# Kernel optimization log

Hardware: AMD Instinct MI355X
Metric: run time of the kernel (lower is better)

The kernel has to match this reference:

```python
import jax, jax.numpy as jnp
import numpy as np

NUM_HEADS = 8
MASK_RATE = 0.5


def setup_inputs() -> dict:
    key = jax.random.key(0)
    ks = jax.random.split(key, 6)
    B, N, C = 8, 1024, 256
    TABLE = 10
    att_embedding = jax.random.normal(ks[0], (B, N, C), dtype=jnp.float32)
    relation_position = jax.random.randint(ks[1], (B, N, N), 0, TABLE, dtype=jnp.int32)
    rel_len = jax.random.randint(ks[2], (B,), 0, 20, dtype=jnp.int32)
    W_qkv = jax.random.normal(ks[3], (C, 3 * C), dtype=jnp.float32) * (1.0 / np.sqrt(C))
    W_proj = jax.random.normal(ks[4], (C, C), dtype=jnp.float32) * (1.0 / np.sqrt(C))
    b_proj = jnp.zeros((C,), dtype=jnp.float32)
    bias_table = jax.random.normal(ks[5], (TABLE, NUM_HEADS), dtype=jnp.float32) * 0.02
    return {
        "att_embedding": att_embedding,
        "relation_position": relation_position,
        "rel_len": rel_len,
        "W_qkv": W_qkv,
        "W_proj": W_proj,
        "b_proj": b_proj,
        "bias_table": bias_table,
    }


def reference(att_embedding, relation_position, rel_len, W_qkv, W_proj, b_proj, bias_table):
    B, N, C = att_embedding.shape
    H = NUM_HEADS
    hd = C // H
    scale = hd ** -0.5

    # QKV projection (no bias): [B,N,3C] -> q,k,v each [B,H,N,hd]
    qkv = (att_embedding @ W_qkv).reshape(B, N, 3, H, hd)
    qkv = jnp.transpose(qkv, (2, 0, 3, 1, 4))
    q, k, v = qkv[0], qkv[1], qkv[2]

    # Attention scores [B,H,N,N]
    attn = jnp.einsum("bhnd,bhmd->bhnm", q, k) * scale

    # Relative position bias: gather [B,N,N,H] -> [B,H,N,N]
    pos_bias = jnp.transpose(bias_table[relation_position], (0, 3, 1, 2))

    # Mask bias: table row t gets -100 iff t > mask_len (mask_len+1 .. TABLE-1);
    # identical across heads -> compute as [B,1,N,N] instead of materializing [B,H,N,N].
    mask_len = (rel_len.astype(jnp.float32) * MASK_RATE).astype(jnp.int32)
    mask_bias = jnp.where(relation_position > mask_len[:, None, None], -100.0, 0.0)[:, None]

    attn = jax.nn.softmax(attn + pos_bias + mask_bias, axis=-1)

    # Weighted values -> [B,N,C] -> output projection
    x = jnp.einsum("bhnm,bhmd->bnhd", attn, v).reshape(B, N, C)
    x = x @ W_proj + b_proj
    return x
```

## Files before the change

kernel.cpp:

```cpp
#include <hip/hip_runtime.h>
#include <hip/hip_bf16.h>

typedef __bf16 bf16;
typedef __bf16 bf16x2 __attribute__((ext_vector_type(2)));
typedef __bf16 bf16x8 __attribute__((ext_vector_type(8)));
typedef float f32x4 __attribute__((ext_vector_type(4)));
typedef int i32x4 __attribute__((ext_vector_type(4)));

#define B_ 8
#define N_ 1024
#define C_ 256
#define H_ 8
#define C3_ 768
#define SCALE 0.17677669529663689f
#define FMAX 16.0f


__global__ __launch_bounds__(256) void prep(
    const float* __restrict__ Wqkv, const float* __restrict__ Wproj,
    bf16* __restrict__ Wq_tiled, bf16* __restrict__ Wp_tiled)
{
  int bb = blockIdx.x;
  int o = bb * 256 + threadIdx.x;
  if (bb < 768) {
    int kk = o & 31;
    int idx = o >> 5;
    int nr = idx & 63;
    int qq = idx >> 6;
    int nt = qq % 12, kt = qq / 12;
    int n = nt * 64 + nr, k = kt * 32 + kk;
    Wq_tiled[o] = (bf16)Wqkv[k * C3_ + n];
  } else {
    int p = o - 768 * 256;
    int kk = p & 31;
    int n = (p >> 5) & 255;
    int kt = p >> 13;
    int k = kt * 32 + kk;
    Wp_tiled[p] = (bf16)Wproj[k * C_ + n];
  }
}

__global__ __launch_bounds__(256) void gemm_qkv(
    const float* __restrict__ A, const bf16* __restrict__ Wq_tiled,
    bf16* __restrict__ q, bf16* __restrict__ kT, bf16* __restrict__ vT)
{
  __shared__ bf16 As[128][40];
  __shared__ bf16 Bts[128][40];
  __shared__ bf16 Vls[64][136];

  int tid = threadIdx.x;
  int wave = tid >> 6, lane = tid & 63, quad = lane >> 4, l16 = lane & 15;
  int m0 = blockIdx.x * 128, n0 = blockIdx.y * 128;
  int msub = (wave & 1) * 64, nsub = (wave >> 1) * 64;

  f32x4 acc[4][4] = {};

  int arow = tid >> 1, akc = (tid & 1) * 16;
  const float* aptr = A + (long)(m0 + arow) * C_ + akc;
  int bn = tid >> 1, bkc = (tid & 1) * 16;
  const bf16* bptr = Wq_tiled +
      ((long)(blockIdx.y * 2 + (bn >> 6)) * 2048 + (bn & 63) * 32 + bkc);

  float4 a0 = *reinterpret_cast<const float4*>(aptr);
  float4 a1 = *reinterpret_cast<const float4*>(aptr + 4);
  float4 a2 = *reinterpret_cast<const float4*>(aptr + 8);
  float4 a3 = *reinterpret_cast<const float4*>(aptr + 12);
  i32x4 bv0 = *reinterpret_cast<const i32x4*>(bptr);
  i32x4 bv1 = *reinterpret_cast<const i32x4*>(bptr + 8);

  for (int kt = 0; kt < 8; ++kt) {
    __syncthreads();
    {
      bf16 at[16] = {(bf16)a0.x, (bf16)a0.y, (bf16)a0.z, (bf16)a0.w,
                     (bf16)a1.x, (bf16)a1.y, (bf16)a1.z, (bf16)a1.w,
                     (bf16)a2.x, (bf16)a2.y, (bf16)a2.z, (bf16)a2.w,
                     (bf16)a3.x, (bf16)a3.y, (bf16)a3.z, (bf16)a3.w};
      *reinterpret_cast<bf16x8*>(&As[arow][akc]) = *reinterpret_cast<bf16x8*>(at);
      *reinterpret_cast<bf16x8*>(&As[arow][akc + 8]) = *reinterpret_cast<bf16x8*>(at + 8);
      *reinterpret_cast<i32x4*>(&Bts[bn][bkc]) = bv0;
      *reinterpret_cast<i32x4*>(&Bts[bn][bkc + 8]) = bv1;
    }
    __syncthreads();

    if (kt < 7) {
      int kn = (kt + 1) * 32;
      a0 = *reinterpret_cast<const float4*>(aptr + kn);
      a1 = *reinterpret_cast<const float4*>(aptr + kn + 4);
      a2 = *reinterpret_cast<const float4*>(aptr + kn + 8);
      a3 = *reinterpret_cast<const float4*>(aptr + kn + 12);
      bv0 = *reinterpret_cast<const i32x4*>(bptr + (long)(kt + 1) * 24576);
      bv1 = *reinterpret_cast<const i32x4*>(bptr + (long)(kt + 1) * 24576 + 8);
    }

    bf16x8 af[4], bfr[4];
#pragma unroll
    for (int mi = 0; mi < 4; ++mi)
      af[mi] = *reinterpret_cast<const bf16x8*>(&As[msub + mi * 16 + l16][quad * 8]);
#pragma unroll
    for (int ni = 0; ni < 4; ++ni)
      bfr[ni] = *reinterpret_cast<const bf16x8*>(&Bts[nsub + ni * 16 + l16][quad * 8]);
#pragma unroll
    for (int mi = 0; mi < 4; ++mi)
#pragma unroll
      for (int ni = 0; ni < 4; ++ni)
        acc[mi][ni] = __builtin_amdgcn_mfma_f32_16x16x32_bf16(af[mi], bfr[ni], acc[mi][ni], 0, 0, 0);
  }

  if (n0 < 256) {
#pragma unroll
    for (int mi = 0; mi < 4; ++mi)
#pragma unroll
      for (int ni = 0; ni < 4; ++ni)
#pragma unroll
        for (int r = 0; r < 4; ++r) {
          int row = m0 + msub + mi * 16 + quad * 4 + r;
          int col = n0 + nsub + ni * 16 + l16;
          q[(long)row * 256 + col] = (bf16)(acc[mi][ni][r] * SCALE);
        }
  } else if (n0 < 512) {
#pragma unroll
    for (int mi = 0; mi < 4; ++mi)
#pragma unroll
      for (int ni = 0; ni < 4; ++ni)
#pragma unroll
        for (int r = 0; r < 4; ++r) {
          int row = m0 + msub + mi * 16 + quad * 4 + r;
          int c = n0 + nsub + ni * 16 + l16 - 256;
          int b = row >> 10, n = row & 1023;
          int h = c >> 5, d = c & 31;
          kT[(((long)(b * H_ + h)) * N_ + n) * 32 + d] = (bf16)acc[mi][ni][r];
        }
  } else {
    int b = m0 >> 10;
#pragma unroll
    for (int ch = 0; ch < 2; ++ch) {
      __syncthreads();
      if ((nsub >> 6) == ch) {
#pragma unroll
        for (int mi = 0; mi < 4; ++mi)
#pragma unroll
          for (int ni = 0; ni < 4; ++ni)
#pragma unroll
            for (int r = 0; r < 4; ++r) {
              int cc = ni * 16 + l16;
              int nn = msub + mi * 16 + quad * 4 + r;
              int np = (nn & 96) | ((nn & 12) << 1) | (nn & 3) | (((nn >> 4) & 1) << 2);
              Vls[cc][np] = (bf16)acc[mi][ni][r];
            }
      }
      __syncthreads();
      int cc = tid >> 2, nseg = (tid & 3) * 32;
      long base = ((long)(b * C_ + (n0 - 512) + ch * 64 + cc)) * N_ + (m0 & 1023) + nseg;
#pragma unroll
      for (int j = 0; j < 4; ++j)
        *reinterpret_cast<i32x4*>(vT + base + j * 8) =
            *reinterpret_cast<const i32x4*>(&Vls[cc][nseg + j * 8]);
    }
  }
}

__global__ __launch_bounds__(512) void flash_attn(
    const bf16* __restrict__ q, const bf16* __restrict__ kT,
    const bf16* __restrict__ vT, const int* __restrict__ rel,
    const int* __restrict__ rel_len, const float* __restrict__ btab,
    const bf16* __restrict__ Wp_tiled, const float* __restrict__ bias,
    float* __restrict__ out)
{
  __shared__ __align__(16) char smem[74240];
  char* KBp = smem;
  char* VBp = smem + 32768;
  char* RBp = smem + 65536;
  float* ebtl = (float*)(smem + 73728);

  int tid = threadIdx.x;
  int h = tid >> 6, lane = tid & 63, quad = lane >> 4, l16 = lane & 15;

  int wg = blockIdx.y * 64 + blockIdx.x;
  int swz = (wg & 7) * 64 + (wg >> 3);
  int b = swz >> 6, i0 = (swz & 63) * 16;
  long bN = (long)b * N_;

  int mask_len = (int)((float)rel_len[b] * 0.5f);
  if (tid < 80) {
    int t = tid >> 3, hh = tid & 7;
    ebtl[hh * 16 + t] = __expf(btab[t * H_ + hh] + (t > mask_len ? -100.f : 0.f) - FMAX);
  }

  bf16x8 qf = *reinterpret_cast<const bf16x8*>(
      q + (bN + i0 + l16) * 256 + h * 32 + quad * 8);

  int l = lane;
  int sxc = (((l & 3) ^ ((l >> 3) & 3)) << 4);
  int kc0 = (l >> 2) * 64 + sxc;
  int vc0 = (h * 32 + (l >> 2)) * 2048 + sxc;
  int i_loc = (h & 3) * 4 + (l >> 4);
  int j_loc = (h >> 2) * 16 + ((((l >> 2) & 3) ^ ((i_loc >> 1) & 3)) << 2) + (l & 3);
  int rc = i_loc * 4096 + j_loc * 4;

  const char* kTb = (const char*)kT + ((long)(b * 8 + h) << 16);
  const char* vTb = (const char*)vT + (long)b * 524288;
  const char* rb0 = (const char*)rel + (bN + i0) * 4096;

  int swq = ((quad ^ ((l16 >> 1) & 3)) << 4);
  int kr = h * 2048 + l16 * 64 + swq;
  int rr = l16 * 64 + swq;

#define GLD16(G, L) __builtin_amdgcn_global_load_lds(                         \
    (const __attribute__((address_space(1))) void*)(G),                       \
    (__attribute__((address_space(3))) void*)(L), 16, 0, 0)
#define GLD4(G, L) __builtin_amdgcn_global_load_lds(                          \
    (const __attribute__((address_space(1))) void*)(G),                       \
    (__attribute__((address_space(3))) void*)(L), 4, 0, 0)

#define GATH(G, R0, R1) do {                                                  \
    _Pragma("unroll")                                                         \
    for (int e = 0; e < 4; ++e) {                                             \
      G[e]     = ebtl[h * 16 + R0[e]];                                        \
      G[4 + e] = ebtl[h * 16 + R1[e]];                                        \
    }                                                                         \
  } while (0)

#define COMP(K0, K1, V0, V1, G) do {                                          \
    f32x4 z = {};                                                             \
    f32x4 s0 = __builtin_amdgcn_mfma_f32_16x16x32_bf16(K0, qf, z, 0, 0, 0);   \
    f32x4 s1 = __builtin_amdgcn_mfma_f32_16x16x32_bf16(K1, qf, z, 0, 0, 0);   \
    bf16x8 pa;                                                                \
    _Pragma("unroll")                                                         \
    for (int e = 0; e < 4; ++e) {                                             \
      float p0 = __expf(s0[e]) * G[e];                                        \
      float p1 = __expf(s1[e]) * G[4 + e];                                    \
      l_acc += p0 + p1;                                                       \
      pa[e] = (bf16)p0;                                                       \
      pa[4 + e] = (bf16)p1;                                                   \
    }                                                                         \
    oacc[0] = __builtin_amdgcn_mfma_f32_16x16x32_bf16(pa, V0, oacc[0], 0, 0, 0); \
    oacc[1] = __builtin_amdgcn_mfma_f32_16x16x32_bf16(pa, V1, oacc[1], 0, 0, 0); \
  } while (0)

#define TILE(TT, BC, BN, BRN, BR3, GC, GN) do {                               \
    int tn_ = ((TT) + 1) & 31, tr_ = ((TT) + 3) & 31;                         \
    GLD16(kTb + tn_ * 2048 + kc0,       KBp + (BN) * 16384 + h * 2048);       \
    GLD16(kTb + tn_ * 2048 + kc0 + 1024, KBp + (BN) * 16384 + h * 2048 + 1024);\
    GLD16(vTb + tn_ * 64 + vc0,         VBp + (BN) * 16384 + h * 2048);       \
    GLD16(vTb + tn_ * 64 + vc0 + 32768, VBp + (BN) * 16384 + h * 2048 + 1024);\
    GLD4(rb0 + tr_ * 128 + rc,          RBp + (BR3) * 2048 + h * 256);        \
    asm volatile("s_waitcnt vmcnt(6)" ::: "memory");                          \
    __builtin_amdgcn_s_barrier();                                             \
    bf16x8 kf0 = *(const bf16x8*)(KBp + (BC) * 16384 + kr);                   \
    bf16x8 kf1 = *(const bf16x8*)(KBp + (BC) * 16384 + kr + 1024);            \
    bf16x8 vf0 = *(const bf16x8*)(VBp + (BC) * 16384 + kr);                   \
    bf16x8 vf1 = *(const bf16x8*)(VBp + (BC) * 16384 + kr + 1024);            \
    i32x4 rv0 = *(const i32x4*)(RBp + (BRN) * 2048 + rr);                     \
    i32x4 rv1 = *(const i32x4*)(RBp + (BRN) * 2048 + rr + 1024);              \
    GATH(GN, rv0, rv1);                                                       \
    COMP(kf0, kf1, vf0, vf1, GC);                                             \
    __builtin_amdgcn_s_barrier();                                             \
  } while (0)

  f32x4 oacc[2] = {};
  float l_acc = 0.f;
  float gA[8], gB[8];

  GLD16(kTb + kc0,        KBp + h * 2048);
  GLD16(kTb + kc0 + 1024, KBp + h * 2048 + 1024);
  GLD16(vTb + vc0,         VBp + h * 2048);
  GLD16(vTb + vc0 + 32768, VBp + h * 2048 + 1024);
  GLD4(rb0 + rc,       RBp + h * 256);
  GLD4(rb0 + 128 + rc, RBp + 2048 + h * 256);
  GLD4(rb0 + 256 + rc, RBp + 4096 + h * 256);
  asm volatile("s_waitcnt vmcnt(2)" ::: "memory");
  __syncthreads();
  {
    i32x4 rv0 = *(const i32x4*)(RBp + rr);
    i32x4 rv1 = *(const i32x4*)(RBp + rr + 1024);
    GATH(gA, rv0, rv1);
  }

#pragma unroll 1
  for (int t = 0; t < 32; t += 4) {
    TILE(t + 0, 0, 1, 1, 3, gA, gB);
    TILE(t + 1, 1, 0, 2, 0, gB, gA);
    TILE(t + 2, 0, 1, 3, 1, gA, gB);
    TILE(t + 3, 1, 0, 0, 2, gB, gA);
  }
#undef TILE
#undef COMP
#undef GATH
#undef GLD16
#undef GLD4

  asm volatile("s_waitcnt vmcnt(0)" ::: "memory");
  __syncthreads();

  float lsum = l_acc;
  lsum += __shfl_xor(lsum, 16);
  lsum += __shfl_xor(lsum, 32);
  float inv = 1.f / lsum;

  bf16 (*attL)[264] = (bf16(*)[264])(void*)smem;
#pragma unroll
  for (int r = 0; r < 4; ++r) {
    float invr = __shfl(inv, quad * 4 + r);
    attL[quad * 4 + r][h * 32 + l16] = (bf16)(oacc[0][r] * invr);
    attL[quad * 4 + r][h * 32 + 16 + l16] = (bf16)(oacc[1][r] * invr);
  }
  __syncthreads();

  f32x4 pacc[2] = {};
  const bf16* wp = Wp_tiled + ((h * 32 + l16) * 32 + quad * 8);
#pragma unroll
  for (int kt = 0; kt < 8; ++kt) {
    bf16x8 afr = *reinterpret_cast<const bf16x8*>(&attL[l16][kt * 32 + quad * 8]);
    bf16x8 b0 = *reinterpret_cast<const bf16x8*>(wp + kt * 8192);
    bf16x8 b1 = *reinterpret_cast<const bf16x8*>(wp + kt * 8192 + 512);
    pacc[0] = __builtin_amdgcn_mfma_f32_16x16x32_bf16(afr, b0, pacc[0], 0, 0, 0);
    pacc[1] = __builtin_amdgcn_mfma_f32_16x16x32_bf16(afr, b1, pacc[1], 0, 0, 0);
  }
  float bi0 = bias[h * 32 + l16];
  float bi1 = bias[h * 32 + 16 + l16];
#pragma unroll
  for (int r = 0; r < 4; ++r) {
    long rowoff = (bN + i0 + quad * 4 + r) * C_ + h * 32;
    out[rowoff + l16] = pacc[0][r] + bi0;
    out[rowoff + 16 + l16] = pacc[1][r] + bi1;
  }
}

extern "C" void kernel_launch(void* const* d_in, const int* in_sizes, int n_in,
                              void* d_out, int out_size, void* d_ws, size_t ws_size,
                              hipStream_t stream) {
  const float* X     = (const float*)d_in[0];
  const int*   rel   = (const int*)d_in[1];
  const int*   rlen  = (const int*)d_in[2];
  const float* Wqkv  = (const float*)d_in[3];
  const float* Wproj = (const float*)d_in[4];
  const float* bproj = (const float*)d_in[5];
  const float* btab  = (const float*)d_in[6];
  float* out = (float*)d_out;

  char* ws = (char*)d_ws;
  bf16* Wq_tiled = (bf16*)ws;
  bf16* Wp_tiled = (bf16*)(ws + 393216);
  bf16* q  = (bf16*)(ws + 524288);
  bf16* kT = (bf16*)(ws + 524288 + 4194304);
  bf16* vT = (bf16*)(ws + 524288 + 2 * 4194304);

  prep<<<dim3(1024), 256, 0, stream>>>(Wqkv, Wproj, Wq_tiled, Wp_tiled);
  gemm_qkv<<<dim3(8192 / 128, C3_ / 128), 256, 0, stream>>>(X, Wq_tiled, q, kT, vT);
  flash_attn<<<dim3(N_ / 16, B_), 512, 0, stream>>>(
      q, kT, vT, rel, rlen, btab, Wp_tiled, bproj, out);
}
```

Before: 136.7 us.

## Pack relation indices to bytes and drop per-tile barriers in flash attention

The prep kernel gains extra blocks that convert the int32 relation_position tensor into a uint8 copy in workspace. The attention kernel then streams one quarter of the bytes for the bias gather, unpacking indices with shifts. Its shared-memory layout is rearranged so each wave only reads the K, V and relation slices it loaded itself. That lets the two block-wide barriers per tile be removed, and the relation buffering becomes a three-slot rotation with a 6-way unrolled loop. The trade-off is an extra full read of the int32 tensor plus a byte write in the prep stage, in exchange for less traffic and less synchronisation in the main loop.

```diff
diff --git a/kernel.cpp b/kernel.cpp
--- a/kernel.cpp
+++ b/kernel.cpp
@@ -18,11 +18,13 @@
 
 __global__ __launch_bounds__(256) void prep(
     const float* __restrict__ Wqkv, const float* __restrict__ Wproj,
-    bf16* __restrict__ Wq_tiled, bf16* __restrict__ Wp_tiled)
+    const int* __restrict__ rel,
+    bf16* __restrict__ Wq_tiled, bf16* __restrict__ Wp_tiled,
+    unsigned char* __restrict__ rel8)
 {
   int bb = blockIdx.x;
-  int o = bb * 256 + threadIdx.x;
   if (bb < 768) {
+    int o = bb * 256 + threadIdx.x;
     int kk = o & 31;
     int idx = o >> 5;
     int nr = idx & 63;
@@ -30,13 +32,25 @@
     int nt = qq % 12, kt = qq / 12;
     int n = nt * 64 + nr, k = kt * 32 + kk;
     Wq_tiled[o] = (bf16)Wqkv[k * C3_ + n];
-  } else {
-    int p = o - 768 * 256;
+  } else if (bb < 1024) {
+    int p = (bb - 768) * 256 + threadIdx.x;
     int kk = p & 31;
     int n = (p >> 5) & 255;
     int kt = p >> 13;
     int k = kt * 32 + kk;
     Wp_tiled[p] = (bf16)Wproj[k * C_ + n];
+  } else {
+    long p = ((long)(bb - 1024) * 256 + threadIdx.x) * 16;
+    i32x4 a = *reinterpret_cast<const i32x4*>(rel + p);
+    i32x4 b2 = *reinterpret_cast<const i32x4*>(rel + p + 4);
+    i32x4 c = *reinterpret_cast<const i32x4*>(rel + p + 8);
+    i32x4 d = *reinterpret_cast<const i32x4*>(rel + p + 12);
+    unsigned o0 = (unsigned)a[0] | ((unsigned)a[1] << 8) | ((unsigned)a[2] << 16) | ((unsigned)a[3] << 24);
+    unsigned o1 = (unsigned)b2[0] | ((unsigned)b2[1] << 8) | ((unsigned)b2[2] << 16) | ((unsigned)b2[3] << 24);
+    unsigned o2 = (unsigned)c[0] | ((unsigned)c[1] << 8) | ((unsigned)c[2] << 16) | ((unsigned)c[3] << 24);
+    unsigned o3 = (unsigned)d[0] | ((unsigned)d[1] << 8) | ((unsigned)d[2] << 16) | ((unsigned)d[3] << 24);
+    i32x4 ov = {(int)o0, (int)o1, (int)o2, (int)o3};
+    *reinterpret_cast<i32x4*>(rel8 + p) = ov;
   }
 }
 
@@ -161,16 +175,16 @@
 
 __global__ __launch_bounds__(512) void flash_attn(
     const bf16* __restrict__ q, const bf16* __restrict__ kT,
-    const bf16* __restrict__ vT, const int* __restrict__ rel,
+    const bf16* __restrict__ vT, const unsigned char* __restrict__ rel8,
     const int* __restrict__ rel_len, const float* __restrict__ btab,
     const bf16* __restrict__ Wp_tiled, const float* __restrict__ bias,
     float* __restrict__ out)
 {
-  __shared__ __align__(16) char smem[74240];
-  char* KBp = smem;
-  char* VBp = smem + 32768;
-  char* RBp = smem + 65536;
-  float* ebtl = (float*)(smem + 73728);
+  __shared__ __align__(16) char smem[78336];
+  char* const KB0 = smem;
+  char* const VB0 = smem + 32768;
+  char* const RB0 = smem + 65536;
+  float* const ebtl = (float*)(smem + 77824);
 
   int tid = threadIdx.x;
   int h = tid >> 6, lane = tid & 63, quad = lane >> 4, l16 = lane & 15;
@@ -189,21 +203,25 @@
   bf16x8 qf = *reinterpret_cast<const bf16x8*>(
       q + (bN + i0 + l16) * 256 + h * 32 + quad * 8);
 
+  __syncthreads();
+
   int l = lane;
   int sxc = (((l & 3) ^ ((l >> 3) & 3)) << 4);
   int kc0 = (l >> 2) * 64 + sxc;
   int vc0 = (h * 32 + (l >> 2)) * 2048 + sxc;
-  int i_loc = (h & 3) * 4 + (l >> 4);
-  int j_loc = (h >> 2) * 16 + ((((l >> 2) & 3) ^ ((i_loc >> 1) & 3)) << 2) + (l & 3);
-  int rc = i_loc * 4096 + j_loc * 4;
+  int rc0 = (l >> 3) * 1024 + (l & 7) * 4;
 
   const char* kTb = (const char*)kT + ((long)(b * 8 + h) << 16);
   const char* vTb = (const char*)vT + (long)b * 524288;
-  const char* rb0 = (const char*)rel + (bN + i0) * 4096;
+  const char* rb8 = (const char*)rel8 + (bN + i0) * 1024;
 
   int swq = ((quad ^ ((l16 >> 1) & 3)) << 4);
   int kr = h * 2048 + l16 * 64 + swq;
-  int rr = l16 * 64 + swq;
+  int rr = h * 512 + l16 * 32 + quad * 4;
+
+#define KB(i) (KB0 + (i) * 16384)
+#define VB(i) (VB0 + (i) * 16384)
+#define RB(i) (RB0 + (i) * 4096)
 
 #define GLD16(G, L) __builtin_amdgcn_global_load_lds(                         \
     (const __attribute__((address_space(1))) void*)(G),                       \
@@ -212,11 +230,11 @@
     (const __attribute__((address_space(1))) void*)(G),                       \
     (__attribute__((address_space(3))) void*)(L), 4, 0, 0)
 
-#define GATH(G, R0, R1) do {                                                  \
+#define GATH(G, RV0, RV1) do {                                                \
     _Pragma("unroll")                                                         \
     for (int e = 0; e < 4; ++e) {                                             \
-      G[e]     = ebtl[h * 16 + R0[e]];                                        \
-      G[4 + e] = ebtl[h * 16 + R1[e]];                                        \
+      G[e]     = ebtl[h * 16 + (int)((RV0 >> (8 * e)) & 255u)];               \
+      G[4 + e] = ebtl[h * 16 + (int)((RV1 >> (8 * e)) & 255u)];               \
     }                                                                         \
   } while (0)
 
@@ -237,57 +255,65 @@
     oacc[1] = __builtin_amdgcn_mfma_f32_16x16x32_bf16(pa, V1, oacc[1], 0, 0, 0); \
   } while (0)
 
-#define TILE(TT, BC, BN, BRN, BR3, GC, GN) do {                               \
-    int tn_ = ((TT) + 1) & 31, tr_ = ((TT) + 3) & 31;                         \
-    GLD16(kTb + tn_ * 2048 + kc0,       KBp + (BN) * 16384 + h * 2048);       \
-    GLD16(kTb + tn_ * 2048 + kc0 + 1024, KBp + (BN) * 16384 + h * 2048 + 1024);\
-    GLD16(vTb + tn_ * 64 + vc0,         VBp + (BN) * 16384 + h * 2048);       \
-    GLD16(vTb + tn_ * 64 + vc0 + 32768, VBp + (BN) * 16384 + h * 2048 + 1024);\
-    GLD4(rb0 + tr_ * 128 + rc,          RBp + (BR3) * 2048 + h * 256);        \
-    asm volatile("s_waitcnt vmcnt(6)" ::: "memory");                          \
-    __builtin_amdgcn_s_barrier();                                             \
-    bf16x8 kf0 = *(const bf16x8*)(KBp + (BC) * 16384 + kr);                   \
-    bf16x8 kf1 = *(const bf16x8*)(KBp + (BC) * 16384 + kr + 1024);            \
-    bf16x8 vf0 = *(const bf16x8*)(VBp + (BC) * 16384 + kr);                   \
-    bf16x8 vf1 = *(const bf16x8*)(VBp + (BC) * 16384 + kr + 1024);            \
-    i32x4 rv0 = *(const i32x4*)(RBp + (BRN) * 2048 + rr);                     \
-    i32x4 rv1 = *(const i32x4*)(RBp + (BRN) * 2048 + rr + 1024);              \
+#define TILE(T_, KVR, KVW, RR_, RW_, GC, GN) do {                             \
+    int tn_ = ((T_) + 1) & 31, tr_ = ((T_) + 3) & 31;                         \
+    GLD16(kTb + tn_ * 2048 + kc0,        KB(KVW) + h * 2048);                 \
+    GLD16(kTb + tn_ * 2048 + kc0 + 1024, KB(KVW) + h * 2048 + 1024);          \
+    GLD16(vTb + tn_ * 64 + vc0,          VB(KVW) + h * 2048);                 \
+    GLD16(vTb + tn_ * 64 + vc0 + 32768,  VB(KVW) + h * 2048 + 1024);          \
+    GLD4(rb8 + tr_ * 32 + rc0,           RB(RW_) + h * 512);                  \
+    GLD4(rb8 + tr_ * 32 + rc0 + 8192,    RB(RW_) + h * 512 + 256);            \
+    asm volatile("s_waitcnt vmcnt(8)" ::: "memory");                          \
+    bf16x8 kf0 = *(const bf16x8*)(KB(KVR) + kr);                              \
+    bf16x8 kf1 = *(const bf16x8*)(KB(KVR) + kr + 1024);                       \
+    bf16x8 vf0 = *(const bf16x8*)(VB(KVR) + kr);                              \
+    bf16x8 vf1 = *(const bf16x8*)(VB(KVR) + kr + 1024);                       \
+    unsigned rv0 = *(const unsigned*)(RB(RR_) + rr);                          \
+    unsigned rv1 = *(const unsigned*)(RB(RR_) + rr + 16);                     \
     GATH(GN, rv0, rv1);                                                       \
     COMP(kf0, kf1, vf0, vf1, GC);                                             \
-    __builtin_amdgcn_s_barrier();                                             \
   } while (0)
 
   f32x4 oacc[2] = {};
   float l_acc = 0.f;
   float gA[8], gB[8];
 
-  GLD16(kTb + kc0,        KBp + h * 2048);
-  GLD16(kTb + kc0 + 1024, KBp + h * 2048 + 1024);
-  GLD16(vTb + vc0,         VBp + h * 2048);
-  GLD16(vTb + vc0 + 32768, VBp + h * 2048 + 1024);
-  GLD4(rb0 + rc,       RBp + h * 256);
-  GLD4(rb0 + 128 + rc, RBp + 2048 + h * 256);
-  GLD4(rb0 + 256 + rc, RBp + 4096 + h * 256);
+  GLD16(kTb + kc0,        KB(0) + h * 2048);
+  GLD16(kTb + kc0 + 1024, KB(0) + h * 2048 + 1024);
+  GLD16(vTb + vc0,          VB(0) + h * 2048);
+  GLD16(vTb + vc0 + 32768,  VB(0) + h * 2048 + 1024);
+  GLD4(rb8 + rc0,             RB(0) + h * 512);
+  GLD4(rb8 + rc0 + 8192,      RB(0) + h * 512 + 256);
+  GLD4(rb8 + 32 + rc0,        RB(1) + h * 512);
+  GLD4(rb8 + 32 + rc0 + 8192, RB(1) + h * 512 + 256);
+  GLD4(rb8 + 64 + rc0,        RB(2) + h * 512);
+  GLD4(rb8 + 64 + rc0 + 8192, RB(2) + h * 512 + 256);
   asm volatile("s_waitcnt vmcnt(2)" ::: "memory");
-  __syncthreads();
   {
-    i32x4 rv0 = *(const i32x4*)(RBp + rr);
-    i32x4 rv1 = *(const i32x4*)(RBp + rr + 1024);
+    unsigned rv0 = *(const unsigned*)(RB(0) + rr);
+    unsigned rv1 = *(const unsigned*)(RB(0) + rr + 16);
     GATH(gA, rv0, rv1);
   }
 
 #pragma unroll 1
-  for (int t = 0; t < 32; t += 4) {
-    TILE(t + 0, 0, 1, 1, 3, gA, gB);
-    TILE(t + 1, 1, 0, 2, 0, gB, gA);
-    TILE(t + 2, 0, 1, 3, 1, gA, gB);
-    TILE(t + 3, 1, 0, 0, 2, gB, gA);
-  }
+  for (int t = 0; t < 30; t += 6) {
+    TILE(t + 0, 0, 1, 1, 0, gA, gB);
+    TILE(t + 1, 1, 0, 2, 1, gB, gA);
+    TILE(t + 2, 0, 1, 0, 2, gA, gB);
+    TILE(t + 3, 1, 0, 1, 0, gB, gA);
+    TILE(t + 4, 0, 1, 2, 1, gA, gB);
+    TILE(t + 5, 1, 0, 0, 2, gB, gA);
+  }
+  TILE(30, 0, 1, 1, 0, gA, gB);
+  TILE(31, 1, 0, 2, 1, gB, gA);
 #undef TILE
 #undef COMP
 #undef GATH
 #undef GLD16
 #undef GLD4
+#undef KB
+#undef VB
+#undef RB
 
   asm volatile("s_waitcnt vmcnt(0)" ::: "memory");
   __syncthreads();
@@ -344,9 +370,10 @@
   bf16* q  = (bf16*)(ws + 524288);
   bf16* kT = (bf16*)(ws + 524288 + 4194304);
   bf16* vT = (bf16*)(ws + 524288 + 2 * 4194304);
-
-  prep<<<dim3(1024), 256, 0, stream>>>(Wqkv, Wproj, Wq_tiled, Wp_tiled);
+  unsigned char* rel8 = (unsigned char*)(ws + 13107200);
+
+  prep<<<dim3(3072), 256, 0, stream>>>(Wqkv, Wproj, rel, Wq_tiled, Wp_tiled, rel8);
   gemm_qkv<<<dim3(8192 / 128, C3_ / 128), 256, 0, stream>>>(X, Wq_tiled, q, kT, vT);
   flash_attn<<<dim3(N_ / 16, B_), 512, 0, stream>>>(
-      q, kT, vT, rel, rlen, btab, Wp_tiled, bproj, out);
+      q, kT, vT, rel8, rlen, btab, Wp_tiled, bproj, out);
 }
```

Measured after the change: 140.6 us. +2.9%, slower.
